# Optimization experiments

Measured on AMD Instinct MI355X. Metric: run time of the kernel, lower is better.

Reference implementation:

```python
import jax, jax.numpy as jnp
import numpy as np

INPUT_WIDTH = 256
STATE_WIDTH = 1792
OUTPUT_WIDTH = 256
STREAM_WIDTH = INPUT_WIDTH + STATE_WIDTH  # 2048
LINEARITY = 0.99999
SEQ, BATCH = 512, 256


def setup_inputs() -> dict:
    key = jax.random.key(0)
    ks = jax.random.split(key, 4)
    # xavier-ish / kaiming-ish scales for the two square Linears
    w1_scale = (6.0 / (STREAM_WIDTH + STREAM_WIDTH)) ** 0.5
    w2_scale = (2.0 / STREAM_WIDTH) ** 0.5
    return {
        "x": jax.random.normal(ks[0], (SEQ, BATCH, INPUT_WIDTH), jnp.float32),
        "initial_state": jax.random.normal(ks[1], (STATE_WIDTH,), jnp.float32),
        "W1": jax.random.normal(ks[2], (STREAM_WIDTH, STREAM_WIDTH), jnp.float32) * w1_scale,
        "b1": jnp.zeros((STREAM_WIDTH,), jnp.float32),
        "W2": jax.random.normal(ks[3], (STREAM_WIDTH, STREAM_WIDTH), jnp.float32) * w2_scale,
        "b2": jnp.zeros((STREAM_WIDTH,), jnp.float32),
    }


def reference(x, initial_state, W1, b1, W2, b2):
    # ResRnn.forward with state=None, seq_indices=-1 (defaults).
    seq, batch, _ = x.shape
    # stream starts as (1 - linearity) * initial_state; ShiftRight keeps only
    # the first STATE_WIDTH columns of the carried stream, so we carry a full
    # (batch, STREAM_WIDTH) stream whose trailing INPUT_WIDTH cols are unused
    # on the first step.
    s0 = (1.0 - LINEARITY) * initial_state  # (STATE_WIDTH,)
    carry0 = jnp.concatenate(
        [jnp.broadcast_to(s0, (batch, STATE_WIDTH)),
         jnp.zeros((batch, INPUT_WIDTH), x.dtype)], axis=-1)

    def step(stream, xt):
        # ShiftRight: new stream head = current input, tail = old stream prefix
        s = jnp.concatenate([xt, stream[:, :STATE_WIDTH]], axis=-1)  # (B, 2048)
        # Res: Linear -> ReLU -> Linear with heavy residual mixing
        h = jnp.maximum(s @ W1.T + b1, 0.0)
        out = LINEARITY * s + (1.0 - LINEARITY) * (h @ W2.T + b2)
        return out, None

    final, _ = jax.lax.scan(step, carry0, x)
    # seq_indices=-1 -> last timestep's stream for every batch element
    outputs = final[..., -OUTPUT_WIDTH:]   # (B, OUTPUT_WIDTH)
    states = final[..., :-OUTPUT_WIDTH]    # (B, STREAM_WIDTH - OUTPUT_WIDTH)
    return outputs, states
```

## Files before the change

### kernel.cpp

```cpp
#include <hip/hip_runtime.h>
#include <hip/hip_bf16.h>
#include <stdint.h>

#define SEQ  512
#define NB   256
#define SW   2048
#define STW  1792
#define INW  256
#define LINC 0.99999f

typedef float f32x4 __attribute__((ext_vector_type(4)));

#define WS_ABORT 2048
#define WS_XF8   16384
#define XF8SLOT  131072
#define WS_W1F8  (2*1024*1024)
#define WS_W2F8  (6*1024*1024)
#define WS_H8    (10*1024*1024)
#define H8SLOT   524288


__device__ __forceinline__ unsigned ald32(const void* p){
  return __hip_atomic_load((const unsigned*)p, __ATOMIC_RELAXED, __HIP_MEMORY_SCOPE_AGENT);
}
__device__ __forceinline__ void ast64(void* p, uint64_t v){
  __hip_atomic_store((uint64_t*)p, v, __ATOMIC_RELAXED, __HIP_MEMORY_SCOPE_AGENT);
}
__device__ __forceinline__ void ast32(void* p, unsigned v){
  __hip_atomic_store((unsigned*)p, v, __ATOMIC_RELAXED, __HIP_MEMORY_SCOPE_AGENT);
}

__device__ __forceinline__ uint64_t pack8(const float* f){
  int lo = 0, hi = 0;
  lo = __builtin_amdgcn_cvt_pk_fp8_f32(f[0], f[1], lo, false);
  lo = __builtin_amdgcn_cvt_pk_fp8_f32(f[2], f[3], lo, true);
  hi = __builtin_amdgcn_cvt_pk_fp8_f32(f[4], f[5], hi, false);
  hi = __builtin_amdgcn_cvt_pk_fp8_f32(f[6], f[7], hi, true);
  return (uint64_t)(uint32_t)lo | ((uint64_t)(uint32_t)hi << 32);
}
__device__ __forceinline__ uint64_t pack8v(float4 a, float4 b){
  int lo = 0, hi = 0;
  lo = __builtin_amdgcn_cvt_pk_fp8_f32(a.x, a.y, lo, false);
  lo = __builtin_amdgcn_cvt_pk_fp8_f32(a.z, a.w, lo, true);
  hi = __builtin_amdgcn_cvt_pk_fp8_f32(b.x, b.y, hi, false);
  hi = __builtin_amdgcn_cvt_pk_fp8_f32(b.z, b.w, hi, true);
  return (uint64_t)(uint32_t)lo | ((uint64_t)(uint32_t)hi << 32);
}
__device__ __forceinline__ f32x4 mf(uint64_t a, long b, f32x4 c){
  return __builtin_amdgcn_mfma_f32_16x16x32_fp8_fp8((long)a, b, c, 0, 0, 0);
}

__device__ __forceinline__ void waitflags(unsigned* flags, unsigned tgt, int prod,
                                          unsigned* abortf, int* s_dead)
{
  if (*s_dead) return;
  long long start = clock64(); int it = 0;
  for (;;){
    unsigned f = (prod >= 0) ? ald32(flags + prod) : tgt;
    if (__ballot(f >= tgt) == ~0ull) break;
    if (((++it) & 15) == 0){
      if (ald32(abortf) != 0u){ *s_dead = 1; break; }
      if (clock64() - start > 40000000LL){ ast32(abortf, 1u); *s_dead = 1; break; }
    }
    __builtin_amdgcn_s_sleep(1);
  }
}

__global__ __launch_bounds__(512, 2)
void fusedA(const float* __restrict__ x, const float* __restrict__ W1,
            const float* __restrict__ W2, const float* __restrict__ b1,
            uint8_t* __restrict__ ws)
{
  __shared__ uint8_t Wl[131072];
  __shared__ uint8_t xfer8[16384];
  __shared__ int s_dead;
  const int blk = blockIdx.x;
  const int tt  = blk >> 5, cq = blk & 31;
  const int tid = threadIdx.x, lane = tid & 63, wv = tid >> 6, l15 = lane & 15;
  const int s0  = wv*2;

  unsigned* flags  = (unsigned*)ws;
  unsigned* abortf = (unsigned*)(ws + WS_ABORT);
  if (tid == 0) s_dead = 0;

  if (tid < 256){
    const bool isw2 = blk >= 128;
    const int unit  = blk & 127;
    const int sc = unit >> 1, hf = unit & 1;
    uint8_t* dstb = ws + (isw2 ? WS_W2F8 : WS_W1F8) + (size_t)sc*65536;
    const int jc  = (tid >> 4) + hf*16;
    const int kc0 = (tid & 15) * 8;
    const float* r = (isw2 ? W2 : W1) + (size_t)(sc*32 + jc)*SW;
    #pragma unroll
    for (int p = 0; p < 16; ++p){
      const int k = kc0 + p*128;
      const int dst = (k >> 5)*1024 + (jc >> 4)*512
                    + (((jc & 15) + (((k >> 3) & 3) << 4)) << 3);
      uint64_t v = pack8v(*(const float4*)(r + k), *(const float4*)(r + k + 4));
      if (isw2) *(uint64_t*)(dstb + dst) = v;
      else      ast64(dstb + dst, v);
    }
  } else if (blk < 60){
    const int tid2 = tid - 256;
    const int u = blk >> 2, q = blk & 3;
    uint8_t* dst = ws + WS_XF8 + (size_t)u*XF8SLOT;
    #pragma unroll
    for (int rr = 0; rr < 8; ++rr){
      const int linear = rr*256 + tid2;
      const int stl = linear >> 9;
      const int rem = linear & 511;
      const int c = rem >> 6, l = rem & 63;
      const int st = q*4 + stl;
      const int row = st*16 + (l & 15);
      const int col = c*32 + ((l >> 4) << 3);
      const float* xp = x + ((size_t)(497 + u)*NB + row)*INW + col;
      float vv[8];
      *(float4*)&vv[0] = *(const float4*)xp;
      *(float4*)&vv[4] = *(const float4*)(xp + 4);
      ast64(dst + (size_t)(st*8 + c)*512 + l*8, pack8(vv));
    }
  }
  __syncthreads();
  if (tid == 0) ast32(&flags[blk], 1u);

  int prod = -1;
  if (lane < 32)      prod = 4*tt + lane;
  else if (lane < 36) prod = 4*cq + (lane - 32);
  waitflags(flags, 1u, prod, abortf, &s_dead);
  asm volatile("" ::: "memory");

  {
    const uint64_t* src = (const uint64_t*)(ws + WS_W1F8 + (size_t)(cq*2)*65536);
    uint64_t* dst = (uint64_t*)Wl;
    #pragma unroll
    for (int k = 0; k < 32; ++k) dst[tid + k*512] = src[tid + k*512];
  }
  float b1v[4];
  #pragma unroll
  for (int f = 0; f < 4; ++f) b1v[f] = b1[cq*64 + f*16 + l15];
  __syncthreads();

  const uint8_t* xf = ws + WS_XF8 + lane*8;
  f32x4 acc[2][4] = {};
  for (int c0 = 0; c0 < 64; c0 += 8){
    const int j = c0 >> 3;
    const uint8_t* slot = xf + (size_t)(7 + tt - j)*XF8SLOT;
    uint64_t a0[8], a1[8];
    #pragma unroll
    for (int i = 0; i < 8; ++i){
      a0[i] = *(const uint64_t*)(slot + (size_t)( s0     *8 + i)*512);
      a1[i] = *(const uint64_t*)(slot + (size_t)((s0 + 1)*8 + i)*512);
    }
    #pragma unroll
    for (int i = 0; i < 8; ++i){
      const uint8_t* bp = Wl + (size_t)(c0 + i)*1024 + lane*8;
      #pragma unroll
      for (int f = 0; f < 4; ++f){
        long b = *(const long*)(bp + (f >> 1)*65536 + (f & 1)*512);
        acc[0][f] = mf(a0[i], b, acc[0][f]);
        acc[1][f] = mf(a1[i], b, acc[1][f]);
      }
    }
  }

  #pragma unroll
  for (int s = 0; s < 2; ++s)
    #pragma unroll
    for (int f = 0; f < 4; ++f)
      #pragma unroll
      for (int i = 0; i < 4; ++i){
        const int row = (s0 + s)*16 + ((lane >> 4) << 2) + i;
        float h = fmaxf(acc[s][f][i] + b1v[f], 0.f);
        int pk = __builtin_amdgcn_cvt_pk_fp8_f32(h, 0.f, 0, false);
        xfer8[row*64 + f*16 + l15] = (uint8_t)(pk & 0xFF);
      }
  __syncthreads();
  uint8_t* h8 = ws + WS_H8 + (size_t)tt*H8SLOT;
  #pragma unroll
  for (int r = 0; r < 4; ++r){
    const int slot = tid + r*512;
    const int st = slot >> 7, cc = (slot >> 6) & 1, l = slot & 63;
    uint64_t v = *(const uint64_t*)
      &xfer8[(st*16 + (l & 15))*64 + cc*32 + ((l >> 4) << 3)];
    *(uint64_t*)(h8 + (size_t)(st*64 + cq*2 + cc)*512 + l*8) = v;
  }
}

__global__ __launch_bounds__(256, 2)
void corrB(const float* __restrict__ x, const float* __restrict__ b2,
           float* __restrict__ out, uint8_t* __restrict__ ws)
{
  __shared__ uint8_t Wl[65536];
  const int blk = blockIdx.x;
  const int unit = blk >> 1, h = blk & 1;
  int j = 0, base = 0;
  while (unit - base >= 64 - 8*j){ base += 64 - 8*j; ++j; }
  const int cb = unit - base;
  const int tt = 7 - j;
  const int tid = threadIdx.x, lane = tid & 63, wv = tid >> 6, l15 = lane & 15;
  const int s0 = h*8 + wv*2;

  {
    const uint64_t* src = (const uint64_t*)(ws + WS_W2F8 + (size_t)cb*65536);
    uint64_t* dst = (uint64_t*)Wl;
    #pragma unroll
    for (int k = 0; k < 32; ++k) dst[tid + k*256] = src[tid + k*256];
  }
  const float b2v0 = b2[cb*32 + l15];
  const float b2v1 = b2[cb*32 + 16 + l15];
  __syncthreads();

  const uint8_t* h8 = ws + WS_H8 + (size_t)tt*H8SLOT + lane*8;
  const uint8_t* A0 = h8 + (size_t)( s0     *64)*512;
  const uint8_t* A1 = h8 + (size_t)((s0 + 1)*64)*512;

  f32x4 acc[2][2] = {{{0,0,0,0},{0,0,0,0}},{{0,0,0,0},{0,0,0,0}}};
  for (int c0 = 0; c0 < 64; c0 += 8){
    uint64_t a0[8], a1[8];
    #pragma unroll
    for (int i = 0; i < 8; ++i){
      a0[i] = *(const uint64_t*)(A0 + (size_t)(c0 + i)*512);
      a1[i] = *(const uint64_t*)(A1 + (size_t)(c0 + i)*512);
    }
    #pragma unroll
    for (int i = 0; i < 8; ++i){
      const uint8_t* bp = Wl + (size_t)(c0 + i)*1024 + lane*8;
      long b0 = *(const long*)bp, b1q = *(const long*)(bp + 512);
      acc[0][0] = mf(a0[i], b0,  acc[0][0]);
      acc[0][1] = mf(a0[i], b1q, acc[0][1]);
      acc[1][0] = mf(a1[i], b0,  acc[1][0]);
      acc[1][1] = mf(a1[i], b1q, acc[1][1]);
    }
  }

  const float UM = (float)(1.0 - 0.99999);
  float linp[9]; linp[0] = 1.f;
  #pragma unroll
  for (int p = 1; p < 9; ++p) linp[p] = linp[p-1]*LINC;
  const float cj = UM * linp[j];

  #pragma unroll
  for (int s = 0; s < 2; ++s)
    #pragma unroll
    for (int f = 0; f < 2; ++f)
      #pragma unroll
      for (int i = 0; i < 4; ++i){
        const int row = (s0 + s)*16 + ((lane >> 4) << 2) + i;
        const int cl  = cb*32 + f*16 + l15;
        const int c   = cl + 256*j;
        float contrib = cj * (acc[s][f][i] + (f ? b2v1 : b2v0));
        if (cb < 8)
          contrib += linp[j+1] * x[((size_t)(511 - j)*NB + row)*INW + cl];
        float* addr = (c < STW) ? out + NB*INW + (size_t)row*STW + c
                                : out + (size_t)row*INW + (c - STW);
        atomicAdd(addr, contrib);
      }
}

extern "C" void kernel_launch(void* const* d_in, const int* in_sizes, int n_in,
                              void* d_out, int out_size, void* d_ws, size_t ws_size,
                              hipStream_t stream)
{
  const float* x   = (const float*)d_in[0];
  const float* W1  = (const float*)d_in[2];
  const float* b1  = (const float*)d_in[3];
  const float* W2  = (const float*)d_in[4];
  const float* b2  = (const float*)d_in[5];
  float* out  = (float*)d_out;
  uint8_t* ws = (uint8_t*)d_ws;

  hipMemsetAsync(ws, 0, 4096, stream);
  hipMemsetAsync(d_out, 0, (size_t)out_size*4, stream);
  hipLaunchKernelGGL(fusedA, dim3(256), dim3(512), 0, stream, x, W1, W2, b1, ws);
  hipLaunchKernelGGL(corrB,  dim3(576), dim3(256), 0, stream, x, b2, out, ws);
}
```

Before: 74.00 us.

## Split prep into its own kernel and replace output memset with flagged stores

Moves the FP8 weight and input conversion out of the fused kernel into a separate prep launch, which removes the inter-block flag spin-wait in the first GEMM kernel. The full output memset is dropped. In the second kernel, j==0 blocks now plain-store their result, with the x term folded in, and raise a flag. The other blocks spin on that flag before doing their atomicAdds. This trades one extra kernel launch and an intra-kernel dependency for less memset and cross-block waiting, and it depends on the j==0 blocks being scheduled first to avoid a deadlock or timeout.

```diff
diff --git a/kernel.cpp b/kernel.cpp
--- a/kernel.cpp
+++ b/kernel.cpp
@@ -11,7 +11,7 @@
 
 typedef float f32x4 __attribute__((ext_vector_type(4)));
 
-#define WS_ABORT 2048
+#define WS_ABORT 512
 #define WS_XF8   16384
 #define XF8SLOT  131072
 #define WS_W1F8  (2*1024*1024)
@@ -22,9 +22,6 @@
 
 __device__ __forceinline__ unsigned ald32(const void* p){
   return __hip_atomic_load((const unsigned*)p, __ATOMIC_RELAXED, __HIP_MEMORY_SCOPE_AGENT);
-}
-__device__ __forceinline__ void ast64(void* p, uint64_t v){
-  __hip_atomic_store((uint64_t*)p, v, __ATOMIC_RELAXED, __HIP_MEMORY_SCOPE_AGENT);
 }
 __device__ __forceinline__ void ast32(void* p, unsigned v){
   __hip_atomic_store((unsigned*)p, v, __ATOMIC_RELAXED, __HIP_MEMORY_SCOPE_AGENT);
@@ -50,40 +47,12 @@
   return __builtin_amdgcn_mfma_f32_16x16x32_fp8_fp8((long)a, b, c, 0, 0, 0);
 }
 
-__device__ __forceinline__ void waitflags(unsigned* flags, unsigned tgt, int prod,
-                                          unsigned* abortf, int* s_dead)
-{
-  if (*s_dead) return;
-  long long start = clock64(); int it = 0;
-  for (;;){
-    unsigned f = (prod >= 0) ? ald32(flags + prod) : tgt;
-    if (__ballot(f >= tgt) == ~0ull) break;
-    if (((++it) & 15) == 0){
-      if (ald32(abortf) != 0u){ *s_dead = 1; break; }
-      if (clock64() - start > 40000000LL){ ast32(abortf, 1u); *s_dead = 1; break; }
-    }
-    __builtin_amdgcn_s_sleep(1);
-  }
-}
-
-__global__ __launch_bounds__(512, 2)
-void fusedA(const float* __restrict__ x, const float* __restrict__ W1,
-            const float* __restrict__ W2, const float* __restrict__ b1,
-            uint8_t* __restrict__ ws)
-{
-  __shared__ uint8_t Wl[131072];
-  __shared__ uint8_t xfer8[16384];
-  __shared__ int s_dead;
-  const int blk = blockIdx.x;
-  const int tt  = blk >> 5, cq = blk & 31;
-  const int tid = threadIdx.x, lane = tid & 63, wv = tid >> 6, l15 = lane & 15;
-  const int s0  = wv*2;
-
-  unsigned* flags  = (unsigned*)ws;
-  unsigned* abortf = (unsigned*)(ws + WS_ABORT);
-  if (tid == 0) s_dead = 0;
-
-  if (tid < 256){
+__global__ __launch_bounds__(256)
+void prep(const float* __restrict__ x, const float* __restrict__ W1,
+          const float* __restrict__ W2, uint8_t* __restrict__ ws)
+{
+  const int blk = blockIdx.x, tid = threadIdx.x;
+  if (blk < 256){
     const bool isw2 = blk >= 128;
     const int unit  = blk & 127;
     const int sc = unit >> 1, hf = unit & 1;
@@ -96,17 +65,16 @@
       const int k = kc0 + p*128;
       const int dst = (k >> 5)*1024 + (jc >> 4)*512
                     + (((jc & 15) + (((k >> 3) & 3) << 4)) << 3);
-      uint64_t v = pack8v(*(const float4*)(r + k), *(const float4*)(r + k + 4));
-      if (isw2) *(uint64_t*)(dstb + dst) = v;
-      else      ast64(dstb + dst, v);
-    }
-  } else if (blk < 60){
-    const int tid2 = tid - 256;
-    const int u = blk >> 2, q = blk & 3;
+      *(uint64_t*)(dstb + dst) =
+        pack8v(*(const float4*)(r + k), *(const float4*)(r + k + 4));
+    }
+  } else {
+    const int unit = blk - 256;
+    const int u = unit >> 2, q = unit & 3;
     uint8_t* dst = ws + WS_XF8 + (size_t)u*XF8SLOT;
     #pragma unroll
     for (int rr = 0; rr < 8; ++rr){
-      const int linear = rr*256 + tid2;
+      const int linear = rr*256 + tid;
       const int stl = linear >> 9;
       const int rem = linear & 511;
       const int c = rem >> 6, l = rem & 63;
@@ -117,17 +85,20 @@
       float vv[8];
       *(float4*)&vv[0] = *(const float4*)xp;
       *(float4*)&vv[4] = *(const float4*)(xp + 4);
-      ast64(dst + (size_t)(st*8 + c)*512 + l*8, pack8(vv));
-    }
-  }
-  __syncthreads();
-  if (tid == 0) ast32(&flags[blk], 1u);
-
-  int prod = -1;
-  if (lane < 32)      prod = 4*tt + lane;
-  else if (lane < 36) prod = 4*cq + (lane - 32);
-  waitflags(flags, 1u, prod, abortf, &s_dead);
-  asm volatile("" ::: "memory");
+      *(uint64_t*)(dst + (size_t)(st*8 + c)*512 + l*8) = pack8(vv);
+    }
+  }
+}
+
+__global__ __launch_bounds__(512, 2)
+void hk2(const float* __restrict__ b1, uint8_t* __restrict__ ws)
+{
+  __shared__ uint8_t Wl[131072];
+  __shared__ uint8_t xfer8[16384];
+  const int blk = blockIdx.x;
+  const int tt  = blk >> 5, cq = blk & 31;
+  const int tid = threadIdx.x, lane = tid & 63, wv = tid >> 6, l15 = lane & 15;
+  const int s0  = wv*2;
 
   {
     const uint64_t* src = (const uint64_t*)(ws + WS_W1F8 + (size_t)(cq*2)*65536);
@@ -187,18 +158,26 @@
 }
 
 __global__ __launch_bounds__(256, 2)
-void corrB(const float* __restrict__ x, const float* __restrict__ b2,
-           float* __restrict__ out, uint8_t* __restrict__ ws)
+void corrAsk(const float* __restrict__ x, const float* __restrict__ b2,
+             float* __restrict__ out, uint8_t* __restrict__ ws)
 {
   __shared__ uint8_t Wl[65536];
+  __shared__ int s_dead;
   const int blk = blockIdx.x;
-  const int unit = blk >> 1, h = blk & 1;
-  int j = 0, base = 0;
-  while (unit - base >= 64 - 8*j){ base += 64 - 8*j; ++j; }
-  const int cb = unit - base;
+  int j, cb, h;
+  if (blk < 128){ j = 0; cb = blk >> 1; h = blk & 1; }
+  else {
+    int b2i = blk - 128, base = 0; j = 1;
+    while (b2i - base >= 2*(64 - 8*j)){ base += 2*(64 - 8*j); ++j; }
+    const int rem = b2i - base; cb = rem >> 1; h = rem & 1;
+  }
   const int tt = 7 - j;
   const int tid = threadIdx.x, lane = tid & 63, wv = tid >> 6, l15 = lane & 15;
   const int s0 = h*8 + wv*2;
+
+  unsigned* flags  = (unsigned*)ws;
+  unsigned* abortf = (unsigned*)(ws + WS_ABORT);
+  if (tid == 0) s_dead = 0;
 
   {
     const uint64_t* src = (const uint64_t*)(ws + WS_W2F8 + (size_t)cb*65536);
@@ -239,22 +218,53 @@
   for (int p = 1; p < 9; ++p) linp[p] = linp[p-1]*LINC;
   const float cj = UM * linp[j];
 
-  #pragma unroll
-  for (int s = 0; s < 2; ++s)
-    #pragma unroll
-    for (int f = 0; f < 2; ++f)
-      #pragma unroll
-      for (int i = 0; i < 4; ++i){
-        const int row = (s0 + s)*16 + ((lane >> 4) << 2) + i;
-        const int cl  = cb*32 + f*16 + l15;
-        const int c   = cl + 256*j;
-        float contrib = cj * (acc[s][f][i] + (f ? b2v1 : b2v0));
-        if (cb < 8)
-          contrib += linp[j+1] * x[((size_t)(511 - j)*NB + row)*INW + cl];
-        float* addr = (c < STW) ? out + NB*INW + (size_t)row*STW + c
-                                : out + (size_t)row*INW + (c - STW);
-        atomicAdd(addr, contrib);
+  if (j == 0){
+    const int J = cb >> 3;
+    const float xw = linp[J + 1];
+    #pragma unroll
+    for (int s = 0; s < 2; ++s)
+      #pragma unroll
+      for (int f = 0; f < 2; ++f)
+        #pragma unroll
+        for (int i = 0; i < 4; ++i){
+          const int row = (s0 + s)*16 + ((lane >> 4) << 2) + i;
+          const int c   = cb*32 + f*16 + l15;
+          float v = cj * (acc[s][f][i] + (f ? b2v1 : b2v0))
+                  + xw * x[((size_t)(511 - J)*NB + row)*INW + (c & 255)];
+          float* addr = (c < STW) ? out + NB*INW + (size_t)row*STW + c
+                                  : out + (size_t)row*INW + (c - STW);
+          ast32(addr, __float_as_uint(v));
+        }
+    __syncthreads();
+    if (tid == 0) ast32(&flags[(cb << 1) | h], 1u);
+  } else {
+    if (!s_dead){
+      const unsigned* fp = flags + (((cb + 8*j) << 1) | h);
+      long long start = clock64(); int it = 0;
+      for (;;){
+        if (__ballot(ald32(fp) >= 1u) == ~0ull) break;
+        if (((++it) & 15) == 0){
+          if (ald32(abortf) != 0u){ if (tid == 0) s_dead = 1; break; }
+          if (clock64() - start > 40000000LL){ ast32(abortf, 1u); break; }
+        }
+        __builtin_amdgcn_s_sleep(1);
       }
+    }
+    asm volatile("" ::: "memory");
+    #pragma unroll
+    for (int s = 0; s < 2; ++s)
+      #pragma unroll
+      for (int f = 0; f < 2; ++f)
+        #pragma unroll
+        for (int i = 0; i < 4; ++i){
+          const int row = (s0 + s)*16 + ((lane >> 4) << 2) + i;
+          const int c   = cb*32 + f*16 + l15 + 256*j;
+          float contrib = cj * (acc[s][f][i] + (f ? b2v1 : b2v0));
+          float* addr = (c < STW) ? out + NB*INW + (size_t)row*STW + c
+                                  : out + (size_t)row*INW + (c - STW);
+          atomicAdd(addr, contrib);
+        }
+  }
 }
 
 extern "C" void kernel_launch(void* const* d_in, const int* in_sizes, int n_in,
@@ -269,8 +279,8 @@
   float* out  = (float*)d_out;
   uint8_t* ws = (uint8_t*)d_ws;
 
-  hipMemsetAsync(ws, 0, 4096, stream);
-  hipMemsetAsync(d_out, 0, (size_t)out_size*4, stream);
-  hipLaunchKernelGGL(fusedA, dim3(256), dim3(512), 0, stream, x, W1, W2, b1, ws);
-  hipLaunchKernelGGL(corrB,  dim3(576), dim3(256), 0, stream, x, b2, out, ws);
-}
+  (void)hipMemsetAsync(ws, 0, 1024, stream);
+  hipLaunchKernelGGL(prep,    dim3(316), dim3(256), 0, stream, x, W1, W2, ws);
+  hipLaunchKernelGGL(hk2,     dim3(256), dim3(512), 0, stream, b1, ws);
+  hipLaunchKernelGGL(corrAsk, dim3(576), dim3(256), 0, stream, x, b2, out, ws);
+}
```

New measurement: 68.16 us. -7.9%, faster.
